# Kernel optimization log

Measured on AMD Instinct MI355X. Metric: run time of the kernel, lower is better.

The kernel has to match this reference:

```python
import jax, jax.numpy as jnp
import numpy as np

INPUT_DIM = 23
LSTM_DIM = 128
HID = 64            # lstm_dim // 2 per direction
MAMBA_DIM = 128
D_INNER = 256       # expand * d_model
D_STATE = 64
D_CONV = 4
DT_RANK = 8         # ceil(d_model / 16)
NUM_LAYERS = 4
SEQ, BATCH = 2048, 4


def setup_inputs() -> dict:
    key = jax.random.key(0)
    ks = iter(jax.random.split(key, 40))
    def rn(shape, s=0.05):
        return jax.random.normal(next(ks), shape, jnp.float32) * s
    inp = {}
    inp["x"] = jax.random.normal(next(ks), (SEQ, BATCH, INPUT_DIM), jnp.float32)
    # 4-layer bidirectional LSTM params (PyTorch layout: W_ih [4H, in], W_hh [4H, H])
    inp["lstm_Wih0"] = rn((2, 4 * HID, INPUT_DIM))
    inp["lstm_WihR"] = rn((NUM_LAYERS - 1, 2, 4 * HID, LSTM_DIM))
    inp["lstm_Whh"] = rn((NUM_LAYERS, 2, 4 * HID, HID))
    inp["lstm_bih"] = rn((NUM_LAYERS, 2, 4 * HID))
    inp["lstm_bhh"] = rn((NUM_LAYERS, 2, 4 * HID))
    # mamba input projection Linear(input_dim, mamba_dim)
    inp["mproj_W"] = rn((MAMBA_DIM, INPUT_DIM))
    inp["mproj_b"] = rn((MAMBA_DIM,))
    # Mamba block params
    inp["in_proj_W"] = rn((2 * D_INNER, MAMBA_DIM))
    inp["conv_w"] = rn((D_INNER, 1, D_CONV))
    inp["conv_b"] = rn((D_INNER,))
    inp["x_proj_W"] = rn((DT_RANK + 2 * D_STATE, D_INNER))
    inp["dt_W"] = rn((D_INNER, DT_RANK))
    inp["dt_b"] = rn((D_INNER,))
    inp["A_log"] = jnp.tile(jnp.log(jnp.arange(1.0, D_STATE + 1.0, dtype=jnp.float32))[None, :], (D_INNER, 1))
    inp["D_skip"] = jnp.ones((D_INNER,), jnp.float32)
    inp["out_proj_W"] = rn((MAMBA_DIM, D_INNER))
    # gate: LayerNorm(lstm_dim + mamba_dim) -> Linear(-> 1) -> sigmoid
    inp["gate_ln_w"] = jnp.ones((LSTM_DIM + MAMBA_DIM,), jnp.float32)
    inp["gate_ln_b"] = jnp.zeros((LSTM_DIM + MAMBA_DIM,), jnp.float32)
    inp["gate_W"] = rn((1, LSTM_DIM + MAMBA_DIM))
    inp["gate_b"] = rn((1,))
    return inp


def _lstm_dir(x, Wih, Whh, b, reverse):
    # x: [L, B, in]; one direction of one LSTM layer. PyTorch gate order i,f,g,o.
    h0 = jnp.zeros((x.shape[1], Whh.shape[1]), x.dtype)
    def step(carry, xt):
        h, c = carry
        g = xt @ Wih.T + h @ Whh.T + b
        i, f, gg, o = jnp.split(g, 4, axis=-1)
        c = jax.nn.sigmoid(f) * c + jax.nn.sigmoid(i) * jnp.tanh(gg)
        h = jax.nn.sigmoid(o) * jnp.tanh(c)
        return (h, c), h
    _, hs = jax.lax.scan(step, (h0, h0), x, reverse=reverse)
    return hs


def _lstm(x, Wih0, WihR, Whh, bih, bhh):
    out = x
    for l in range(NUM_LAYERS):
        Wf = Wih0[0] if l == 0 else WihR[l - 1, 0]
        Wb = Wih0[1] if l == 0 else WihR[l - 1, 1]
        hf = _lstm_dir(out, Wf, Whh[l, 0], bih[l, 0] + bhh[l, 0], False)
        hb = _lstm_dir(out, Wb, Whh[l, 1], bih[l, 1] + bhh[l, 1], True)
        out = jnp.concatenate([hf, hb], axis=-1)  # [L, B, 2H]
    return out


def _mamba(x, in_proj_W, conv_w, conv_b, x_proj_W, dt_W, dt_b, A_log, D_skip, out_proj_W):
    # x: [L, B, d_model]; time axis = 0
    L = x.shape[0]
    xi, z = jnp.split(x @ in_proj_W.T, 2, axis=-1)          # [L,B,d_inner] each
    xp = jnp.pad(xi, ((D_CONV - 1, 0), (0, 0), (0, 0)))      # causal depthwise conv
    conv = conv_b + sum(xp[k:k + L] * conv_w[:, 0, k] for k in range(D_CONV))
    xc = jax.nn.silu(conv)
    dbc = xc @ x_proj_W.T                                    # [L,B,dt_rank+2*d_state]
    dt, Bm, Cm = jnp.split(dbc, [DT_RANK, DT_RANK + D_STATE], axis=-1)
    dt = jax.nn.softplus(dt @ dt_W.T + dt_b)                 # [L,B,d_inner]
    A = -jnp.exp(A_log)                                      # [d_inner,d_state]
    def step(h, inp):
        dt_t, B_t, C_t, x_t = inp
        h = jnp.exp(dt_t[..., None] * A) * h + dt_t[..., None] * B_t[:, None, :] * x_t[..., None]
        return h, jnp.einsum('bds,bs->bd', h, C_t)
    h0 = jnp.zeros((x.shape[1], D_INNER, D_STATE), x.dtype)
    _, ys = jax.lax.scan(step, h0, (dt, Bm, Cm, xc))          # ys: [L,B,d_inner]
    y = (ys + xc * D_skip) * jax.nn.silu(z)
    return y @ out_proj_W.T                                   # [L,B,d_model]


def _forward(x, lstm_Wih0, lstm_WihR, lstm_Whh, lstm_bih, lstm_bhh, mproj_W, mproj_b,
             in_proj_W, conv_w, conv_b, x_proj_W, dt_W, dt_b, A_log, D_skip, out_proj_W,
             gate_ln_w, gate_ln_b, gate_W, gate_b):
    lstm_out = _lstm(x, lstm_Wih0, lstm_WihR, lstm_Whh, lstm_bih, lstm_bhh)  # [L,B,128]
    mamba_out = _mamba(x @ mproj_W.T + mproj_b, in_proj_W, conv_w, conv_b,
                       x_proj_W, dt_W, dt_b, A_log, D_skip, out_proj_W)      # [L,B,128]
    comb = jnp.concatenate([lstm_out, mamba_out], axis=-1)                   # [L,B,256]
    mu = comb.mean(-1, keepdims=True)
    var = comb.var(-1, keepdims=True)
    ln = (comb - mu) / jnp.sqrt(var + 1e-5) * gate_ln_w + gate_ln_b
    gate = jax.nn.sigmoid(ln @ gate_W.T + gate_b)                            # [L,B,1]
    return gate * lstm_out + (1.0 - gate) * mamba_out


def reference(x, lstm_Wih0, lstm_WihR, lstm_Whh, lstm_bih, lstm_bhh, mproj_W, mproj_b,
              in_proj_W, conv_w, conv_b, x_proj_W, dt_W, dt_b, A_log, D_skip, out_proj_W,
              gate_ln_w, gate_ln_b, gate_W, gate_b):
    return _forward(x, lstm_Wih0, lstm_WihR, lstm_Whh, lstm_bih, lstm_bhh, mproj_W, mproj_b,
                    in_proj_W, conv_w, conv_b, x_proj_W, dt_W, dt_b, A_log, D_skip, out_proj_W,
                    gate_ln_w, gate_ln_b, gate_W, gate_b)
```

## Files before the change

### kernel.cpp

```cpp
#include <hip/hip_runtime.h>

#define SEQ   2048
#define NM    8192

typedef __attribute__((ext_vector_type(4))) float f4;
typedef _Float16 f16x8 __attribute__((ext_vector_type(8)));

__device__ __forceinline__ float frcp(float x){ return __builtin_amdgcn_rcpf(x); }
__device__ __forceinline__ float sigm(float x){ return frcp(1.f + __expf(-x)); }
__device__ __forceinline__ float tanhf_(float x){ return 1.f - 2.f*frcp(__expf(2.f*x) + 1.f); }
__device__ __forceinline__ f4 mfma16h(f16x8 a, f16x8 b, f4 c){
  return __builtin_amdgcn_mfma_f32_16x16x32_f16(a, b, c, 0, 0, 0);
}
__device__ __forceinline__ void barrier_lds_only(){
  asm volatile("s_waitcnt lgkmcnt(0)\n\ts_barrier" ::: "memory");
}

__global__ __launch_bounds__(256) void gemm_k(
    const float* __restrict__ A, int lda,
    const float* __restrict__ W0, const float* __restrict__ W1, int Nhalf,
    const float* __restrict__ b0a, const float* __restrict__ b0b,
    const float* __restrict__ b1a, const float* __restrict__ b1b,
    float* __restrict__ out, int M, int N, int K, int mode)
{
  __shared__ alignas(16) float As[16][68];
  __shared__ alignas(16) float Ws[16][68];
  const int tid = threadIdx.x;
  const int tn = tid & 15, tm = tid >> 4;
  const int n0 = blockIdx.x * 64, m0 = blockIdx.y * 64;
  const int srow = tid >> 2, sk = (tid & 3) * 4;
  float acc[4][4] = {};
  for (int k0 = 0; k0 < K; k0 += 16) {
    const int am = m0 + srow;
    #pragma unroll
    for (int q = 0; q < 4; ++q) {
      int k = k0 + sk + q;
      As[sk + q][srow] = (k < K) ? A[(size_t)am * lda + k] : 0.f;
    }
    const int wn = n0 + srow;
    const float* Wp = W0; int nn = wn;
    if (W1 != nullptr && wn >= Nhalf) { Wp = W1; nn = wn - Nhalf; }
    #pragma unroll
    for (int q = 0; q < 4; ++q) {
      int k = k0 + sk + q;
      Ws[sk + q][srow] = (wn < N && k < K) ? Wp[(size_t)nn * K + k] : 0.f;
    }
    __syncthreads();
    #pragma unroll
    for (int k = 0; k < 16; ++k) {
      f4 a = *(const f4*)&As[k][tm*4];
      f4 w = *(const f4*)&Ws[k][tn*4];
      #pragma unroll
      for (int i = 0; i < 4; ++i)
        #pragma unroll
        for (int j = 0; j < 4; ++j) acc[i][j] += a[i]*w[j];
    }
    __syncthreads();
  }
  #pragma unroll
  for (int i = 0; i < 4; ++i) {
    #pragma unroll
    for (int j = 0; j < 4; ++j) {
      int m = m0 + tm*4 + i, n = n0 + tn*4 + j;
      if (n >= N) continue;
      float bias = 0.f;
      if (n < Nhalf) { if (b0a) bias += b0a[n]; if (b0b) bias += b0b[n]; }
      else { if (b1a) bias += b1a[n - Nhalf]; if (b1b) bias += b1b[n - Nhalf]; }
      float v = acc[i][j] + bias;
      if (mode == 2) {
        int dd = n >> 8, r = n & 255, t = m >> 2, b = m & 3;
        int gate = r >> 6, jj = r & 63;
        int tq = dd ? (SEQ - 1 - t) : t;
        out[((size_t)(dd*SEQ + tq) * 4 + b) * 256 + (jj << 2) + gate] = v;
      } else {
        out[(size_t)m * N + n] = v;
      }
    }
  }
}

__global__ __launch_bounds__(256) void wcomb_k(
    const float* __restrict__ inprojW, const float* __restrict__ mprojW,
    const float* __restrict__ mprojB, float* __restrict__ wc,
    float* __restrict__ bvec)
{
  int idx = blockIdx.x * 256 + threadIdx.x;
  if (idx >= 512 * 24) return;
  int n = idx / 24, c = idx % 24;
  const float* wi = inprojW + (size_t)n * 128;
  float s = 0.f;
  if (c < 23) {
    for (int k = 0; k < 128; ++k) s += wi[k] * mprojW[k*23 + c];
    wc[n*23 + c] = s;
  } else {
    for (int k = 0; k < 128; ++k) s += wi[k] * mprojB[k];
    bvec[n] = s;
  }
}

__global__ __launch_bounds__(256) void moutproj_k(
    const float* __restrict__ z, const float* __restrict__ ys,
    const float* __restrict__ xc, const float* __restrict__ Dsk,
    const float* __restrict__ Wp, float* __restrict__ out)
{
  __shared__ alignas(16) float As[16][68];
  __shared__ alignas(16) float Ws[16][68];
  const int tid = threadIdx.x;
  const int tn = tid & 15, tm = tid >> 4;
  const int n0 = blockIdx.x * 64, m0 = blockIdx.y * 64;
  const int srow = tid >> 2, sk = (tid & 3) * 4;
  float acc[4][4] = {};
  for (int k0 = 0; k0 < 256; k0 += 16) {
    #pragma unroll
    for (int q = 0; q < 4; ++q) {
      int k = k0 + sk + q;
      size_t idx = (size_t)(m0 + srow) * 256 + k;
      float zz = z[idx];
      As[sk + q][srow] = (ys[idx] + xc[idx]*Dsk[k]) * zz * sigm(zz);
      Ws[sk + q][srow] = Wp[(size_t)(n0 + srow) * 256 + k];
    }
    __syncthreads();
    #pragma unroll
    for (int k = 0; k < 16; ++k) {
      f4 a = *(const f4*)&As[k][tm*4];
      f4 w = *(const f4*)&Ws[k][tn*4];
      #pragma unroll
      for (int i = 0; i < 4; ++i)
        #pragma unroll
        for (int j = 0; j < 4; ++j) acc[i][j] += a[i]*w[j];
    }
    __syncthreads();
  }
  #pragma unroll
  for (int i = 0; i < 4; ++i)
    #pragma unroll
    for (int j = 0; j < 4; ++j)
      out[(size_t)(m0 + tm*4 + i) * 128 + n0 + tn*4 + j] = acc[i][j];
}

__global__ __launch_bounds__(256, 1) void fused_k(
    int stage,
    const float* __restrict__ G,
    const float* __restrict__ Whh,
    float* __restrict__ lout,
    const float* __restrict__ rA, int lda,
    const float* __restrict__ rW, const float* __restrict__ rbias,
    float* __restrict__ rout, int ldo, int N, int K,
    const float* __restrict__ dtW, const float* __restrict__ dtB,
    float* __restrict__ dtout,
    const float* __restrict__ mdbc, const float* __restrict__ mdtb,
    const float* __restrict__ mxc, const float* __restrict__ mAlog,
    float* __restrict__ mys)
{
  __shared__ alignas(16) _Float16 hb2[2][4][80];
  __shared__ float As[64][17];
  __shared__ float Ws[64][17];
  __shared__ float dtl[64][8];

  const int tid = threadIdx.x;

  if (blockIdx.x < 2) {
    __builtin_amdgcn_s_setprio(1);
    const int dir = blockIdx.x;
    const int w = tid >> 6, lane = tid & 63;
    const int q = lane >> 4, c = lane & 15;
    const int bb = c & 3, sel = c >> 2;
    const int mtile = 4*sel + w;
    const int jcol = mtile*4 + q;

    for (int i = tid; i < 2*4*80; i += 256) ((_Float16*)hb2)[i] = (_Float16)0.f;

    const float* Gd = G + (size_t)dir * SEQ * 1024;
    const float* Wd = Whh + dir * 256 * 64;

    f16x8 Wf[4][2];
    #pragma unroll
    for (int s2 = 0; s2 < 4; ++s2) {
      const int m = 4*s2 + w;
      const int orow = (c & 3)*64 + m*4 + (c >> 2);
      #pragma unroll
      for (int kt = 0; kt < 2; ++kt) {
        const float* src = Wd + orow*64 + kt*32 + q*8;
        #pragma unroll
        for (int e = 0; e < 8; ++e) Wf[s2][kt][e] = (_Float16)src[e];
      }
    }

    float cc = 0.f;

    auto loadG = [&](int t) -> f4 {
      return *(const f4*)(Gd + (((size_t)t*4 + bb) << 8) + mtile*16 + q*4);
    };
    f4 gp[8];
    #pragma unroll
    for (int i = 0; i < 8; ++i) gp[i] = loadG(i);
    __syncthreads();

    auto step = [&](int t, f4 gv) {
      const int p0 = t & 1, p1 = p0 ^ 1;
      const f16x8 h0 = *(const f16x8*)&hb2[p0][bb][q*8];
      const f16x8 h1 = *(const f16x8*)&hb2[p0][bb][32 + q*8];
      f4 a0 = mfma16h(Wf[0][0], h0, gv); a0 = mfma16h(Wf[0][1], h1, a0);
      f4 a1 = mfma16h(Wf[1][0], h0, gv); a1 = mfma16h(Wf[1][1], h1, a1);
      f4 a2 = mfma16h(Wf[2][0], h0, gv); a2 = mfma16h(Wf[2][1], h1, a2);
      f4 a3 = mfma16h(Wf[3][0], h0, gv); a3 = mfma16h(Wf[3][1], h1, a3);
      const bool sb0 = (sel & 1) != 0, sb1 = (sel & 2) != 0;
      f4 g4;
      #pragma unroll
      for (int r = 0; r < 4; ++r) {
        float x01 = sb0 ? a1[r] : a0[r];
        float x23 = sb0 ? a3[r] : a2[r];
        g4[r] = sb1 ? x23 : x01;
      }
      cc = sigm(g4[1])*cc + sigm(g4[0])*tanhf_(g4[2]);
      const float hh = sigm(g4[3])*tanhf_(cc);
      hb2[p1][bb][jcol] = (_Float16)hh;
      const int to = dir ? (SEQ-1 - t) : t;
      lout[((size_t)to*4 + bb)*128 + dir*64 + jcol] = hh;
      barrier_lds_only();
    };

    for (int t0 = 0; t0 < SEQ; t0 += 8) {
      #pragma unroll
      for (int i = 0; i < 8; ++i) {
        step(t0 + i, gp[i]);
        if (t0 + 8 + i < SEQ) gp[i] = loadG(t0 + 8 + i);
      }
    }
    return;
  }

  int rb = blockIdx.x - 2;

  if (stage == 1) {
    int idx = rb*256 + tid;
    int d = idx & 255, m2 = idx >> 8;
    int t = m2 >> 2, b = m2 & 3;
    float s = rbias[d];
    #pragma unroll
    for (int k = 0; k < 4; ++k) {
      int tt = t - 3 + k;
      if (tt >= 0) s += rA[(size_t)((tt*4 + b) << 8) + d] * rW[d*4 + k];
    }
    rout[idx] = s * sigm(s);
    return;
  }

  if (stage == 3) {
    const int wid = rb*4 + (tid >> 6);
    const int lane = tid & 63;
    const int b = wid >> 8, d = wid & 255;
    const float Av = -__expf(mAlog[d*64 + lane]);
    const float* pB  = mdbc + (size_t)b*136 + 8 + lane;
    const float* pC  = mdbc + (size_t)b*136 + 72 + lane;
    const float* pdt = mdtb + (size_t)b*256 + d;
    const float* px  = mxc  + (size_t)b*256 + d;
    float* py = mys + (size_t)b*256 + d;
    float h = 0.f;
    float Bv = pB[0], Cv = pC[0], dtv = pdt[0], xv = px[0];
    #pragma unroll 2
    for (int t = 0; t < SEQ; ++t) {
      float Bn = 0.f, Cn = 0.f, dtn = 0.f, xn = 0.f;
      if (t + 1 < SEQ) {
        size_t od = (size_t)(t+1) * 544;
        size_t ox = (size_t)(t+1) * 1024;
        Bn = pB[od]; Cn = pC[od]; dtn = pdt[ox]; xn = px[ox];
      }
      float a = __expf(dtv * Av);
      h = a*h + (dtv*xv)*Bv;
      float p = h * Cv;
      #pragma unroll
      for (int mm = 1; mm < 64; mm <<= 1) p += __shfl_xor(p, mm, 64);
      if (lane == 0) py[(size_t)t * 1024] = p;
      Bv = Bn; Cv = Cn; dtv = dtn; xv = xn;
    }
    return;
  }

  const float* gW = rW; const float* gB = rbias; float* gO = rout;
  if (stage == 0 && rb >= 512) { rb -= 512; gW = dtW; gB = dtB; gO = dtout; }
  const int ntiles = (N + 63) >> 6;
  const int nt = rb % ntiles, mt = rb / ntiles;
  const int n0 = nt * 64, m0 = mt * 64;
  const int tn = tid & 15, tm = tid >> 4;
  const int srow = tid >> 2, sk = (tid & 3) * 4;
  float acc[4][4] = {};
  for (int k0 = 0; k0 < K; k0 += 16) {
    #pragma unroll
    for (int qq = 0; qq < 4; ++qq) {
      int k = k0 + sk + qq;
      As[srow][sk + qq] = (k < K) ? rA[(size_t)(m0 + srow) * lda + k] : 0.f;
      Ws[srow][sk + qq] = (n0 + srow < N && k < K) ? gW[(size_t)(n0 + srow) * K + k] : 0.f;
    }
    __syncthreads();
    #pragma unroll
    for (int k = 0; k < 16; ++k) {
      float a[4], w[4];
      #pragma unroll
      for (int i = 0; i < 4; ++i) a[i] = As[tm*4+i][k];
      #pragma unroll
      for (int j = 0; j < 4; ++j) w[j] = Ws[tn*4+j][k];
      #pragma unroll
      for (int i = 0; i < 4; ++i)
        #pragma unroll
        for (int j = 0; j < 4; ++j) acc[i][j] += a[i]*w[j];
    }
    __syncthreads();
  }
  #pragma unroll
  for (int i = 0; i < 4; ++i) {
    #pragma unroll
    for (int j = 0; j < 4; ++j) {
      int m2 = m0 + tm*4 + i, n = n0 + tn*4 + j;
      if (n >= N) continue;
      float v = acc[i][j] + (gB ? gB[n] : 0.f);
      gO[(size_t)m2 * ldo + n] = v;
      if (stage == 2 && nt == 0 && n < 8) dtl[tm*4+i][n] = v;
    }
  }
  if (stage == 2 && nt == 0) {
    __syncthreads();
    for (int idx = tid; idx < 64*256; idx += 256) {
      int ml = idx >> 8, d = idx & 255;
      float s = dtB[d];
      #pragma unroll
      for (int r = 0; r < 8; ++r) s += dtl[ml][r] * dtW[d*8 + r];
      s = (s > 15.f) ? s : __logf(1.f + __expf(s));
      dtout[(size_t)(m0 + ml)*256 + d] = s;
    }
  }
}

__global__ __launch_bounds__(256) void combine_k(
    const float* __restrict__ lstm, const float* __restrict__ mam,
    const float* __restrict__ lnw, const float* __restrict__ lnb,
    const float* __restrict__ gW, const float* __restrict__ gb,
    float* __restrict__ out)
{
  const int pair = blockIdx.x * 4 + (threadIdx.x >> 6);
  const int lane = threadIdx.x & 63;
  const float2 lv = *(const float2*)(lstm + (size_t)pair*128 + lane*2);
  const float2 mv = *(const float2*)(mam  + (size_t)pair*128 + lane*2);
  float s  = lv.x + lv.y + mv.x + mv.y;
  float sq = lv.x*lv.x + lv.y*lv.y + mv.x*mv.x + mv.y*mv.y;
  #pragma unroll
  for (int mm = 1; mm < 64; mm <<= 1) { s += __shfl_xor(s, mm, 64); sq += __shfl_xor(sq, mm, 64); }
  const float mean = s * (1.f/256.f);
  const float var  = sq * (1.f/256.f) - mean*mean;
  const float inv  = rsqrtf(var + 1e-5f);
  const int c0 = lane*2, c2 = 128 + lane*2;
  float n0 = (lv.x-mean)*inv*lnw[c0]   + lnb[c0];
  float n1 = (lv.y-mean)*inv*lnw[c0+1] + lnb[c0+1];
  float n2 = (mv.x-mean)*inv*lnw[c2]   + lnb[c2];
  float n3 = (mv.y-mean)*inv*lnw[c2+1] + lnb[c2+1];
  float dot = n0*gW[c0] + n1*gW[c0+1] + n2*gW[c2] + n3*gW[c2+1];
  #pragma unroll
  for (int mm = 1; mm < 64; mm <<= 1) dot += __shfl_xor(dot, mm, 64);
  const float gate = sigm(dot + gb[0]);
  float2 o;
  o.x = gate*lv.x + (1.f-gate)*mv.x;
  o.y = gate*lv.y + (1.f-gate)*mv.y;
  *(float2*)(out + (size_t)pair*128 + lane*2) = o;
}

extern "C" void kernel_launch(void* const* d_in, const int* in_sizes, int n_in,
                              void* d_out, int out_size, void* d_ws, size_t ws_size,
                              hipStream_t stream)
{
  const float* x       = (const float*)d_in[0];
  const float* Wih0    = (const float*)d_in[1];
  const float* WihR    = (const float*)d_in[2];
  const float* Whh     = (const float*)d_in[3];
  const float* bih     = (const float*)d_in[4];
  const float* bhh     = (const float*)d_in[5];
  const float* mprojW  = (const float*)d_in[6];
  const float* mprojB  = (const float*)d_in[7];
  const float* inprojW = (const float*)d_in[8];
  const float* convw   = (const float*)d_in[9];
  const float* convb   = (const float*)d_in[10];
  const float* xprojW  = (const float*)d_in[11];
  const float* dtW     = (const float*)d_in[12];
  const float* dtB     = (const float*)d_in[13];
  const float* Alog    = (const float*)d_in[14];
  const float* Dskip   = (const float*)d_in[15];
  const float* outprojW= (const float*)d_in[16];
  const float* lnw     = (const float*)d_in[17];
  const float* lnb     = (const float*)d_in[18];
  const float* gWt     = (const float*)d_in[19];
  const float* gb      = (const float*)d_in[20];

  float* WS = (float*)d_ws;
  const size_t M1 = 1048576;
  float* mamba_out = WS;
  float* P     = WS + M1;
  float* G     = P;
  float* lstmA = P + 4*M1;
  float* lstmB = P + 5*M1;
  float* xi    = P + 6*M1;
  float* dtb   = P + 6*M1;
  float* xc    = P + 8*M1;
  float* dbc   = P + 10*M1;
  float* wc    = P + 10*M1 + (size_t)NM*136;
  float* bvec  = wc + 512*23;
  float* ysb   = P + 11*M1 + M1/4;
  const bool zOK = ws_size >= 65ull*1048576;
  float* zbuf  = zOK ? (P + 13*M1 + M1/4)
                     : (P + 6*M1);
  float* outp  = (float*)d_out;

  dim3 blk(256);

  wcomb_k<<<48, blk, 0, stream>>>(inprojW, mprojW, mprojB, wc, bvec);

  const float* lin = x;
  float* louts[4] = {lstmA, lstmB, lstmA, lstmB};
  for (int l = 0; l < 4; ++l) {
    const float* w0; const float* w1; int K;
    if (l == 0) { w0 = Wih0; w1 = Wih0 + 256*23; K = 23; }
    else {
      w0 = WihR + (size_t)((l-1)*2 + 0)*256*128;
      w1 = WihR + (size_t)((l-1)*2 + 1)*256*128;
      K = 128;
    }
    gemm_k<<<dim3(8,128), blk, 0, stream>>>(lin, K, w0, w1, 256,
        bih + (l*2+0)*256, bhh + (l*2+0)*256,
        bih + (l*2+1)*256, bhh + (l*2+1)*256,
        G, NM, 512, K, 2);
    const float* Wl = Whh + (size_t)l*2*256*64;
    if (l == 0) {
      fused_k<<<2 + (zOK ? 1024 : 512), blk, 0, stream>>>(0, G, Wl, louts[l],
          x, 23, wc, bvec, xi, 256, 256, 23,
          zOK ? (wc + 256*23) : nullptr, zOK ? (bvec + 256) : nullptr,
          zOK ? zbuf : nullptr, nullptr, nullptr, nullptr, nullptr, nullptr);
    } else if (l == 1) {
      fused_k<<<2 + 8192, blk, 0, stream>>>(1, G, Wl, louts[l],
          xi, 0, convw, convb, xc, 0, 0, 0,
          nullptr, nullptr, nullptr, nullptr, nullptr, nullptr, nullptr, nullptr);
    } else if (l == 2) {
      fused_k<<<2 + 384, blk, 0, stream>>>(2, G, Wl, louts[l],
          xc, 256, xprojW, nullptr, dbc, 136, 136, 256,
          dtW, dtB, dtb, nullptr, nullptr, nullptr, nullptr, nullptr);
    } else {
      fused_k<<<2 + 256, blk, 0, stream>>>(3, G, Wl, louts[l],
          nullptr, 0, nullptr, nullptr, nullptr, 0, 0, 0,
          nullptr, nullptr, nullptr, dbc, dtb, xc, Alog, ysb);
    }
    lin = louts[l];
  }

  if (!zOK) {
    gemm_k<<<dim3(4,128), blk, 0, stream>>>(x, 23, wc + 256*23, nullptr, 256,
        bvec + 256, nullptr, nullptr, nullptr, zbuf, NM, 256, 23, 0);
  }
  moutproj_k<<<dim3(2,128), blk, 0, stream>>>(zbuf, ysb, xc, Dskip,
      outprojW, mamba_out);
  combine_k<<<2048, blk, 0, stream>>>(lstmB, mamba_out, lnw, lnb, gWt, gb, outp);
}
```

Before: 2.993 ms.

## Merge both LSTM directions into one block with interleaved MFMA chains

Runs the forward and reverse LSTM recurrences in a single workgroup instead of two. The MFMA chains and gate math of both directions are interleaved so each covers the other's latency, and they share one barrier per step. This frees a block for the concurrent Mamba work and reduces the count of serial barrier-bound blocks. In exchange it doubles per-thread register use for weights and halves the G prefetch depth, which could lengthen each step.

```diff
diff --git a/kernel.cpp b/kernel.cpp
--- a/kernel.cpp
+++ b/kernel.cpp
@@ -152,85 +152,109 @@
     const float* __restrict__ mxc, const float* __restrict__ mAlog,
     float* __restrict__ mys)
 {
-  __shared__ alignas(16) _Float16 hb2[2][4][80];
+  __shared__ alignas(16) _Float16 hb2[2][2][4][80];
   __shared__ float As[64][17];
   __shared__ float Ws[64][17];
   __shared__ float dtl[64][8];
 
   const int tid = threadIdx.x;
 
-  if (blockIdx.x < 2) {
+  if (blockIdx.x < 1) {
     __builtin_amdgcn_s_setprio(1);
-    const int dir = blockIdx.x;
     const int w = tid >> 6, lane = tid & 63;
     const int q = lane >> 4, c = lane & 15;
     const int bb = c & 3, sel = c >> 2;
     const int mtile = 4*sel + w;
     const int jcol = mtile*4 + q;
-
-    for (int i = tid; i < 2*4*80; i += 256) ((_Float16*)hb2)[i] = (_Float16)0.f;
-
-    const float* Gd = G + (size_t)dir * SEQ * 1024;
-    const float* Wd = Whh + dir * 256 * 64;
-
-    f16x8 Wf[4][2];
-    #pragma unroll
-    for (int s2 = 0; s2 < 4; ++s2) {
-      const int m = 4*s2 + w;
-      const int orow = (c & 3)*64 + m*4 + (c >> 2);
-      #pragma unroll
-      for (int kt = 0; kt < 2; ++kt) {
-        const float* src = Wd + orow*64 + kt*32 + q*8;
+    const bool sb0 = (sel & 1) != 0, sb1 = (sel & 2) != 0;
+
+    for (int i = tid; i < 2*2*4*80; i += 256) ((_Float16*)hb2)[i] = (_Float16)0.f;
+
+    f16x8 Wf[2][4][2];
+    #pragma unroll
+    for (int d = 0; d < 2; ++d) {
+      const float* Wd = Whh + d * 256 * 64;
+      #pragma unroll
+      for (int s2 = 0; s2 < 4; ++s2) {
+        const int m = 4*s2 + w;
+        const int orow = (c & 3)*64 + m*4 + (c >> 2);
         #pragma unroll
-        for (int e = 0; e < 8; ++e) Wf[s2][kt][e] = (_Float16)src[e];
+        for (int kt = 0; kt < 2; ++kt) {
+          const float* src = Wd + orow*64 + kt*32 + q*8;
+          #pragma unroll
+          for (int e = 0; e < 8; ++e) Wf[d][s2][kt][e] = (_Float16)src[e];
+        }
       }
     }
 
-    float cc = 0.f;
-
-    auto loadG = [&](int t) -> f4 {
-      return *(const f4*)(Gd + (((size_t)t*4 + bb) << 8) + mtile*16 + q*4);
+    float cc0 = 0.f, cc1 = 0.f;
+
+    auto loadG = [&](int d, int t) -> f4 {
+      return *(const f4*)(G + (size_t)d * SEQ * 1024
+                            + (((size_t)t*4 + bb) << 8) + mtile*16 + q*4);
     };
-    f4 gp[8];
-    #pragma unroll
-    for (int i = 0; i < 8; ++i) gp[i] = loadG(i);
-    __syncthreads();
-
-    auto step = [&](int t, f4 gv) {
+    f4 gp[2][4];
+    #pragma unroll
+    for (int i = 0; i < 4; ++i) { gp[0][i] = loadG(0, i); gp[1][i] = loadG(1, i); }
+    __syncthreads();
+
+    auto step = [&](int t, f4 gv0, f4 gv1) {
       const int p0 = t & 1, p1 = p0 ^ 1;
-      const f16x8 h0 = *(const f16x8*)&hb2[p0][bb][q*8];
-      const f16x8 h1 = *(const f16x8*)&hb2[p0][bb][32 + q*8];
-      f4 a0 = mfma16h(Wf[0][0], h0, gv); a0 = mfma16h(Wf[0][1], h1, a0);
-      f4 a1 = mfma16h(Wf[1][0], h0, gv); a1 = mfma16h(Wf[1][1], h1, a1);
-      f4 a2 = mfma16h(Wf[2][0], h0, gv); a2 = mfma16h(Wf[2][1], h1, a2);
-      f4 a3 = mfma16h(Wf[3][0], h0, gv); a3 = mfma16h(Wf[3][1], h1, a3);
-      const bool sb0 = (sel & 1) != 0, sb1 = (sel & 2) != 0;
-      f4 g4;
+      const f16x8 h00 = *(const f16x8*)&hb2[0][p0][bb][q*8];
+      const f16x8 h01 = *(const f16x8*)&hb2[0][p0][bb][32 + q*8];
+      const f16x8 h10 = *(const f16x8*)&hb2[1][p0][bb][q*8];
+      const f16x8 h11 = *(const f16x8*)&hb2[1][p0][bb][32 + q*8];
+      f4 a00 = mfma16h(Wf[0][0][0], h00, gv0); 
+      f4 a01 = mfma16h(Wf[0][1][0], h00, gv0);
+      f4 a02 = mfma16h(Wf[0][2][0], h00, gv0);
+      f4 a03 = mfma16h(Wf[0][3][0], h00, gv0);
+      f4 a10 = mfma16h(Wf[1][0][0], h10, gv1);
+      f4 a11 = mfma16h(Wf[1][1][0], h10, gv1);
+      f4 a12 = mfma16h(Wf[1][2][0], h10, gv1);
+      f4 a13 = mfma16h(Wf[1][3][0], h10, gv1);
+      a00 = mfma16h(Wf[0][0][1], h01, a00);
+      a01 = mfma16h(Wf[0][1][1], h01, a01);
+      a02 = mfma16h(Wf[0][2][1], h01, a02);
+      a03 = mfma16h(Wf[0][3][1], h01, a03);
+      a10 = mfma16h(Wf[1][0][1], h11, a10);
+      a11 = mfma16h(Wf[1][1][1], h11, a11);
+      a12 = mfma16h(Wf[1][2][1], h11, a12);
+      a13 = mfma16h(Wf[1][3][1], h11, a13);
+      f4 g40, g41;
       #pragma unroll
       for (int r = 0; r < 4; ++r) {
-        float x01 = sb0 ? a1[r] : a0[r];
-        float x23 = sb0 ? a3[r] : a2[r];
-        g4[r] = sb1 ? x23 : x01;
+        float x01 = sb0 ? a01[r] : a00[r];
+        float x23 = sb0 ? a03[r] : a02[r];
+        g40[r] = sb1 ? x23 : x01;
+        float y01 = sb0 ? a11[r] : a10[r];
+        float y23 = sb0 ? a13[r] : a12[r];
+        g41[r] = sb1 ? y23 : y01;
       }
-      cc = sigm(g4[1])*cc + sigm(g4[0])*tanhf_(g4[2]);
-      const float hh = sigm(g4[3])*tanhf_(cc);
-      hb2[p1][bb][jcol] = (_Float16)hh;
-      const int to = dir ? (SEQ-1 - t) : t;
-      lout[((size_t)to*4 + bb)*128 + dir*64 + jcol] = hh;
+      cc0 = sigm(g40[1])*cc0 + sigm(g40[0])*tanhf_(g40[2]);
+      cc1 = sigm(g41[1])*cc1 + sigm(g41[0])*tanhf_(g41[2]);
+      const float hh0 = sigm(g40[3])*tanhf_(cc0);
+      const float hh1 = sigm(g41[3])*tanhf_(cc1);
+      hb2[0][p1][bb][jcol] = (_Float16)hh0;
+      hb2[1][p1][bb][jcol] = (_Float16)hh1;
+      lout[((size_t)t*4 + bb)*128 + jcol] = hh0;
+      lout[((size_t)(SEQ-1 - t)*4 + bb)*128 + 64 + jcol] = hh1;
       barrier_lds_only();
     };
 
-    for (int t0 = 0; t0 < SEQ; t0 += 8) {
-      #pragma unroll
-      for (int i = 0; i < 8; ++i) {
-        step(t0 + i, gp[i]);
-        if (t0 + 8 + i < SEQ) gp[i] = loadG(t0 + 8 + i);
+    for (int t0 = 0; t0 < SEQ; t0 += 4) {
+      #pragma unroll
+      for (int i = 0; i < 4; ++i) {
+        step(t0 + i, gp[0][i], gp[1][i]);
+        if (t0 + 4 + i < SEQ) {
+          gp[0][i] = loadG(0, t0 + 4 + i);
+          gp[1][i] = loadG(1, t0 + 4 + i);
+        }
       }
     }
     return;
   }
 
-  int rb = blockIdx.x - 2;
+  int rb = blockIdx.x - 1;
 
   if (stage == 1) {
     int idx = rb*256 + tid;
@@ -428,20 +452,20 @@
         G, NM, 512, K, 2);
     const float* Wl = Whh + (size_t)l*2*256*64;
     if (l == 0) {
-      fused_k<<<2 + (zOK ? 1024 : 512), blk, 0, stream>>>(0, G, Wl, louts[l],
+      fused_k<<<1 + (zOK ? 1024 : 512), blk, 0, stream>>>(0, G, Wl, louts[l],
           x, 23, wc, bvec, xi, 256, 256, 23,
           zOK ? (wc + 256*23) : nullptr, zOK ? (bvec + 256) : nullptr,
           zOK ? zbuf : nullptr, nullptr, nullptr, nullptr, nullptr, nullptr);
     } else if (l == 1) {
-      fused_k<<<2 + 8192, blk, 0, stream>>>(1, G, Wl, louts[l],
+      fused_k<<<1 + 8192, blk, 0, stream>>>(1, G, Wl, louts[l],
           xi, 0, convw, convb, xc, 0, 0, 0,
           nullptr, nullptr, nullptr, nullptr, nullptr, nullptr, nullptr, nullptr);
     } else if (l == 2) {
-      fused_k<<<2 + 384, blk, 0, stream>>>(2, G, Wl, louts[l],
+      fused_k<<<1 + 384, blk, 0, stream>>>(2, G, Wl, louts[l],
           xc, 256, xprojW, nullptr, dbc, 136, 136, 256,
           dtW, dtB, dtb, nullptr, nullptr, nullptr, nullptr, nullptr);
     } else {
-      fused_k<<<2 + 256, blk, 0, stream>>>(3, G, Wl, louts[l],
+      fused_k<<<1 + 256, blk, 0, stream>>>(3, G, Wl, louts[l],
           nullptr, 0, nullptr, nullptr, nullptr, 0, 0, 0,
           nullptr, nullptr, nullptr, dbc, dtb, xc, Alog, ysb);
     }
```

Result: slower. 4.436 ms (+48.2%).
